# Kernel tuning notes

Hardware: AMD Instinct MI355X
Metric: run time of the kernel (lower is better)

Reference implementation:

```python
import jax, jax.numpy as jnp
import numpy as np

N_NODES = 50000
N_EDGES = 800000
D_IN = 512
D_OUT = 128

def setup_inputs() -> dict:
    key = jax.random.key(0)
    k1, k2, k3, k4, k5, k6 = jax.random.split(key, 6)
    std = 1.0 / np.sqrt(D_OUT)
    x = jax.random.normal(k1, (N_NODES, D_IN), dtype=jnp.float32)
    edge_w = jax.random.uniform(k2, (N_EDGES,), dtype=jnp.float32)
    src = jax.random.randint(k3, (N_EDGES,), 0, N_NODES, dtype=jnp.int32)
    dst = jax.random.randint(k4, (N_EDGES,), 0, N_NODES, dtype=jnp.int32)
    W = jax.random.uniform(k5, (D_IN, D_OUT), minval=-std, maxval=std, dtype=jnp.float32)
    b = jax.random.uniform(k6, (D_OUT,), minval=-std, maxval=std, dtype=jnp.float32)
    return {"x": x, "edge_w": edge_w, "src": src, "dst": dst, "W": W, "b": b}

def reference(x, edge_w, src, dst, W, b):
    # Dense GEMM: [N, D_in] @ [D_in, D_out]
    h = x @ W
    # SpMM with COO adjacency: out[i] = sum_{e: dst[e]==i} edge_w[e] * h[src[e]]
    msg = h[src] * edge_w[:, None]          # [E, D_out]
    agg = jax.ops.segment_sum(msg, dst, num_segments=N_NODES)
    return agg + b
```

## Files before the change

### kernel.cpp

```cpp
#include <hip/hip_runtime.h>
#include <hip/hip_bf16.h>

#define M_NODES  50000
#define D_IN_K   512
#define D_OUT_N  128
#define N_EDGES  800000
#define SCAN_NBLK 49

typedef short  bf16x8 __attribute__((ext_vector_type(8)));
typedef float  f32x4  __attribute__((ext_vector_type(4)));

static __device__ __forceinline__ unsigned short f2bf(float f) {
    unsigned u = __float_as_uint(f);
    unsigned r = u + 0x7FFF + ((u >> 16) & 1);
    return (unsigned short)(r >> 16);
}
static __device__ __forceinline__ float bflo(unsigned q) { return __uint_as_float(q << 16); }
static __device__ __forceinline__ float bfhi(unsigned q) { return __uint_as_float(q & 0xFFFF0000u); }

static __device__ __forceinline__ void gl2lds16(const uint4* g, uint4* l) {
    __builtin_amdgcn_global_load_lds(
        (const __attribute__((address_space(1))) void*)g,
        (__attribute__((address_space(3))) void*)l,
        16, 0, 0);
}

__global__ __launch_bounds__(256) void permw_kernel(const float* __restrict__ W,
                                                    unsigned short* __restrict__ Wp) {
    int tid = blockIdx.x * 256 + threadIdx.x;
    int lane = tid & 63;
    int nt   = (tid >> 6) & 7;
    int kb4  = tid >> 9;
    int n    = nt * 16 + (lane & 15);
    int kbase = kb4 * 32 + ((lane >> 4) & 3) * 8;
    unsigned short frag[8];
#pragma unroll
    for (int j = 0; j < 8; ++j)
        frag[j] = f2bf(W[(size_t)(kbase + j) * D_OUT_N + n]);
    *(uint4*)&Wp[(size_t)tid * 8] = *(const uint4*)frag;
}

__global__ __launch_bounds__(256, 4) void mfma_gemm_hist_kernel(const float* __restrict__ x,
                                                                const uint4* __restrict__ Wp4,
                                                                unsigned short* __restrict__ h,
                                                                const int* __restrict__ dst,
                                                                int* __restrict__ counts) {
    __shared__ uint4 wlds[2][1024];

    const int tid  = threadIdx.x;
    const int wave = tid >> 6;
    const int lane = tid & 63;
    const int m0   = blockIdx.x * 64 + wave * 16;
    const int mrow = lane & 15;
    const int kgrp = lane >> 4;

    const int r0 = m0 + mrow;
    const float* xr0 = x + (size_t)((r0 < M_NODES) ? r0 : M_NODES - 1) * D_IN_K + kgrp * 8;

    f32x4 acc[8];
#pragma unroll
    for (int t = 0; t < 8; ++t) acc[t] = (f32x4){0.f, 0.f, 0.f, 0.f};

#pragma unroll
    for (int i = 0; i < 4; ++i)
        gl2lds16(Wp4 + tid + i * 256, &wlds[0][tid + i * 256]);

    float4 a0 = *(const float4*)(xr0);
    float4 a1 = *(const float4*)(xr0 + 4);

    __syncthreads();

    for (int c = 0; c < 8; ++c) {
        const int pb = c & 1;
        if (c < 7) {
#pragma unroll
            for (int i = 0; i < 4; ++i)
                gl2lds16(Wp4 + (c + 1) * 1024 + tid + i * 256,
                         &wlds[pb ^ 1][tid + i * 256]);
        }
#pragma unroll
        for (int kk = 0; kk < 2; ++kk) {
            const int kb = c * 2 + kk;
            float4 n0, n1;
            if (kb < 15) {
                const float* p = xr0 + (kb + 1) * 32;
                n0 = *(const float4*)(p);
                n1 = *(const float4*)(p + 4);
            }
            union { bf16x8 v; __hip_bfloat162 h2[4]; } cv;
            cv.h2[0] = __float22bfloat162_rn(make_float2(a0.x, a0.y));
            cv.h2[1] = __float22bfloat162_rn(make_float2(a0.z, a0.w));
            cv.h2[2] = __float22bfloat162_rn(make_float2(a1.x, a1.y));
            cv.h2[3] = __float22bfloat162_rn(make_float2(a1.z, a1.w));
            bf16x8 af = cv.v;
#pragma unroll
            for (int nt = 0; nt < 8; ++nt) {
                union { uint4 u; bf16x8 v; } wb;
                wb.u = wlds[pb][kk * 512 + nt * 64 + lane];
                acc[nt] = __builtin_amdgcn_mfma_f32_16x16x32_bf16(af, wb.v, acc[nt], 0, 0, 0);
            }
            if (kb < 15) { a0 = n0; a1 = n1; }
        }
        __syncthreads();
    }

#pragma unroll
    for (int r = 0; r < 4; ++r) {
        int rr = m0 + kgrp * 4 + r;
        if (rr < M_NODES) {
            unsigned short* hp = h + (size_t)rr * D_OUT_N + mrow;
#pragma unroll
            for (int nt = 0; nt < 8; ++nt)
                hp[nt * 16] = f2bf(acc[nt][r]);
        }
    }

    const int epb = (N_EDGES + gridDim.x - 1) / gridDim.x;
    const int e0  = blockIdx.x * epb;
    const int e1  = (e0 + epb < N_EDGES) ? e0 + epb : N_EDGES;
    for (int e = e0 + tid; e < e1; e += 256)
        atomicAdd(&counts[dst[e]], 1);
}

__global__ __launch_bounds__(256) void scan_kernel(const int* __restrict__ counts,
                                                   int* __restrict__ offsets,
                                                   int* __restrict__ cursor,
                                                   int* __restrict__ partials,
                                                   int* __restrict__ flags) {
    __shared__ int wsum[4];
    __shared__ int carry_s;
    const int tid  = threadIdx.x;
    const int lane = tid & 63;
    const int wid  = tid >> 6;
    const int blk  = blockIdx.x;
    const int base = blk * 1024 + tid * 4;

    int v[4];
    if (base + 3 < M_NODES) {
        int4 q = *(const int4*)&counts[base];
        v[0] = q.x; v[1] = q.y; v[2] = q.z; v[3] = q.w;
    } else {
#pragma unroll
        for (int i = 0; i < 4; ++i)
            v[i] = (base + i < M_NODES) ? counts[base + i] : 0;
    }
    int t = v[0] + v[1] + v[2] + v[3];

    int s = t;
#pragma unroll
    for (int d = 1; d < 64; d <<= 1) {
        int u = __shfl_up(s, d, 64);
        if (lane >= d) s += u;
    }
    if (lane == 63) wsum[wid] = s;
    __syncthreads();
    int wbase = 0;
#pragma unroll
    for (int w = 0; w < 4; ++w) wbase += (w < wid) ? wsum[w] : 0;
    int total = wsum[0] + wsum[1] + wsum[2] + wsum[3];

    if (tid == 0) {
        __hip_atomic_store(&partials[blk], total, __ATOMIC_RELAXED, __HIP_MEMORY_SCOPE_AGENT);
        __hip_atomic_store(&flags[blk], 1, __ATOMIC_RELEASE, __HIP_MEMORY_SCOPE_AGENT);
        if (blk == 0) offsets[M_NODES] = N_EDGES;
    }

    if (wid == 0) {
        int val = 0;
        if (lane < blk) {
            while (__hip_atomic_load(&flags[lane], __ATOMIC_ACQUIRE, __HIP_MEMORY_SCOPE_AGENT) == 0) {}
            val = __hip_atomic_load(&partials[lane], __ATOMIC_RELAXED, __HIP_MEMORY_SCOPE_AGENT);
        }
#pragma unroll
        for (int d = 32; d > 0; d >>= 1) val += __shfl_xor(val, d, 64);
        if (lane == 0) carry_s = val;
    }
    __syncthreads();
    const int carry = carry_s;

    int run = carry + wbase + s - t;
#pragma unroll
    for (int i = 0; i < 4; ++i) {
        if (base + i < M_NODES) {
            offsets[base + i] = run;
            cursor[base + i]  = run;
        }
        run += v[i];
    }
}

__global__ __launch_bounds__(256) void fill_kernel(const int* __restrict__ src,
                                                   const int* __restrict__ dst,
                                                   const float* __restrict__ edge_w,
                                                   int* __restrict__ cursor,
                                                   int2* __restrict__ ep) {
    int e = blockIdx.x * blockDim.x + threadIdx.x;
    if (e >= N_EDGES) return;
    int d   = dst[e];
    int pos = atomicAdd(&cursor[d], 1);
    ep[pos] = make_int2(src[e], __float_as_int(edge_w[e]));
}

__global__ __launch_bounds__(256) void gather_kernel(const unsigned short* __restrict__ h,
                                                     const int2* __restrict__ ep,
                                                     const int* __restrict__ offsets,
                                                     const float* __restrict__ b,
                                                     float* __restrict__ out) {
    int t    = blockIdx.x * blockDim.x + threadIdx.x;
    int node = t >> 4;
    int lane = t & 15;
    if (node >= M_NODES) return;
    int beg = offsets[node];
    int end = offsets[node + 1];

    float4 b0 = *(const float4*)&b[lane * 8];
    float4 b1 = *(const float4*)&b[lane * 8 + 4];
    float a[4][8];
#pragma unroll
    for (int u = 0; u < 4; ++u)
#pragma unroll
        for (int c = 0; c < 8; ++c) a[u][c] = 0.f;

    int j = beg;
    for (; j + 4 <= end; j += 4) {
        int2 e0 = ep[j], e1 = ep[j + 1], e2 = ep[j + 2], e3 = ep[j + 3];
        uint4 q0 = *(const uint4*)(h + (size_t)e0.x * D_OUT_N + lane * 8);
        uint4 q1 = *(const uint4*)(h + (size_t)e1.x * D_OUT_N + lane * 8);
        uint4 q2 = *(const uint4*)(h + (size_t)e2.x * D_OUT_N + lane * 8);
        uint4 q3 = *(const uint4*)(h + (size_t)e3.x * D_OUT_N + lane * 8);
        float w0 = __int_as_float(e0.y), w1 = __int_as_float(e1.y);
        float w2 = __int_as_float(e2.y), w3 = __int_as_float(e3.y);
        a[0][0] += w0 * bflo(q0.x);  a[0][1] += w0 * bfhi(q0.x);
        a[0][2] += w0 * bflo(q0.y);  a[0][3] += w0 * bfhi(q0.y);
        a[0][4] += w0 * bflo(q0.z);  a[0][5] += w0 * bfhi(q0.z);
        a[0][6] += w0 * bflo(q0.w);  a[0][7] += w0 * bfhi(q0.w);
        a[1][0] += w1 * bflo(q1.x);  a[1][1] += w1 * bfhi(q1.x);
        a[1][2] += w1 * bflo(q1.y);  a[1][3] += w1 * bfhi(q1.y);
        a[1][4] += w1 * bflo(q1.z);  a[1][5] += w1 * bfhi(q1.z);
        a[1][6] += w1 * bflo(q1.w);  a[1][7] += w1 * bfhi(q1.w);
        a[2][0] += w2 * bflo(q2.x);  a[2][1] += w2 * bfhi(q2.x);
        a[2][2] += w2 * bflo(q2.y);  a[2][3] += w2 * bfhi(q2.y);
        a[2][4] += w2 * bflo(q2.z);  a[2][5] += w2 * bfhi(q2.z);
        a[2][6] += w2 * bflo(q2.w);  a[2][7] += w2 * bfhi(q2.w);
        a[3][0] += w3 * bflo(q3.x);  a[3][1] += w3 * bfhi(q3.x);
        a[3][2] += w3 * bflo(q3.y);  a[3][3] += w3 * bfhi(q3.y);
        a[3][4] += w3 * bflo(q3.z);  a[3][5] += w3 * bfhi(q3.z);
        a[3][6] += w3 * bflo(q3.w);  a[3][7] += w3 * bfhi(q3.w);
    }
    for (; j < end; ++j) {
        int2 e0 = ep[j];
        float w0 = __int_as_float(e0.y);
        uint4 q0 = *(const uint4*)(h + (size_t)e0.x * D_OUT_N + lane * 8);
        a[0][0] += w0 * bflo(q0.x);  a[0][1] += w0 * bfhi(q0.x);
        a[0][2] += w0 * bflo(q0.y);  a[0][3] += w0 * bfhi(q0.y);
        a[0][4] += w0 * bflo(q0.z);  a[0][5] += w0 * bfhi(q0.z);
        a[0][6] += w0 * bflo(q0.w);  a[0][7] += w0 * bfhi(q0.w);
    }

    float4 o0 = make_float4(b0.x + a[0][0] + a[1][0] + a[2][0] + a[3][0],
                            b0.y + a[0][1] + a[1][1] + a[2][1] + a[3][1],
                            b0.z + a[0][2] + a[1][2] + a[2][2] + a[3][2],
                            b0.w + a[0][3] + a[1][3] + a[2][3] + a[3][3]);
    float4 o1 = make_float4(b1.x + a[0][4] + a[1][4] + a[2][4] + a[3][4],
                            b1.y + a[0][5] + a[1][5] + a[2][5] + a[3][5],
                            b1.z + a[0][6] + a[1][6] + a[2][6] + a[3][6],
                            b1.w + a[0][7] + a[1][7] + a[2][7] + a[3][7]);
    float* op = &out[(size_t)node * D_OUT_N + lane * 8];
    *(float4*)op = o0;
    *(float4*)(op + 4) = o1;
}

extern "C" void kernel_launch(void* const* d_in, const int* in_sizes, int n_in,
                              void* d_out, int out_size, void* d_ws, size_t ws_size,
                              hipStream_t stream) {
    const float* x      = (const float*)d_in[0];
    const float* edge_w = (const float*)d_in[1];
    const int*   src    = (const int*)d_in[2];
    const int*   dst    = (const int*)d_in[3];
    const float* W      = (const float*)d_in[4];
    const float* b      = (const float*)d_in[5];
    float* out = (float*)d_out;

    char* wsp = (char*)d_ws;
    unsigned short* h = (unsigned short*)wsp;  wsp += (size_t)M_NODES * D_OUT_N * 2;
    int*   counts   = (int*)wsp;         wsp += (size_t)M_NODES * 4;
    int*   flags    = (int*)wsp;         wsp += 64 * 4;
    int*   cursor   = (int*)wsp;         wsp += (size_t)M_NODES * 4;
    int*   offsets  = (int*)wsp;         wsp += (((size_t)M_NODES + 1) * 4 + 15) & ~15ull;
    int2*  ep       = (int2*)wsp;        wsp += (size_t)N_EDGES * 8;
    unsigned short* Wp = (unsigned short*)wsp; wsp += (size_t)16 * 8 * 64 * 8 * 2;
    int*   partials = (int*)wsp;         wsp += (SCAN_NBLK * 4 + 15) & ~15ull;

    hipMemsetAsync(counts, 0, (size_t)M_NODES * 4 + 64 * 4, stream);
    permw_kernel<<<32, 256, 0, stream>>>(W, Wp);
    mfma_gemm_hist_kernel<<<(M_NODES + 63) / 64, 256, 0, stream>>>(
        x, (const uint4*)Wp, h, dst, counts);
    scan_kernel<<<SCAN_NBLK, 256, 0, stream>>>(counts, offsets, cursor, partials, flags);
    fill_kernel<<<(N_EDGES + 255) / 256, 256, 0, stream>>>(src, dst, edge_w, cursor, ep);
    gather_kernel<<<(int)(((long long)M_NODES * 16 + 255) / 256), 256, 0, stream>>>(
        h, ep, offsets, b, out);
}
```

Before: 293.9 us.

## Load GEMM weight fragments directly into registers instead of LDS double-buffer

```diff
diff --git a/kernel.cpp b/kernel.cpp
--- a/kernel.cpp
+++ b/kernel.cpp
@@ -17,13 +17,6 @@
 }
 static __device__ __forceinline__ float bflo(unsigned q) { return __uint_as_float(q << 16); }
 static __device__ __forceinline__ float bfhi(unsigned q) { return __uint_as_float(q & 0xFFFF0000u); }
-
-static __device__ __forceinline__ void gl2lds16(const uint4* g, uint4* l) {
-    __builtin_amdgcn_global_load_lds(
-        (const __attribute__((address_space(1))) void*)g,
-        (__attribute__((address_space(3))) void*)l,
-        16, 0, 0);
-}
 
 __global__ __launch_bounds__(256) void permw_kernel(const float* __restrict__ W,
                                                     unsigned short* __restrict__ Wp) {
@@ -40,13 +33,11 @@
     *(uint4*)&Wp[(size_t)tid * 8] = *(const uint4*)frag;
 }
 
-__global__ __launch_bounds__(256, 4) void mfma_gemm_hist_kernel(const float* __restrict__ x,
+__global__ __launch_bounds__(256, 3) void mfma_gemm_hist_kernel(const float* __restrict__ x,
                                                                 const uint4* __restrict__ Wp4,
                                                                 unsigned short* __restrict__ h,
                                                                 const int* __restrict__ dst,
                                                                 int* __restrict__ counts) {
-    __shared__ uint4 wlds[2][1024];
-
     const int tid  = threadIdx.x;
     const int wave = tid >> 6;
     const int lane = tid & 63;
@@ -61,47 +52,45 @@
 #pragma unroll
     for (int t = 0; t < 8; ++t) acc[t] = (f32x4){0.f, 0.f, 0.f, 0.f};
 
-#pragma unroll
-    for (int i = 0; i < 4; ++i)
-        gl2lds16(Wp4 + tid + i * 256, &wlds[0][tid + i * 256]);
-
+    const uint4* wp = Wp4 + lane;
+
+    uint4 wcur[8], wnxt[8];
+#pragma unroll
+    for (int nt = 0; nt < 8; ++nt) wcur[nt] = wp[nt * 64];
     float4 a0 = *(const float4*)(xr0);
     float4 a1 = *(const float4*)(xr0 + 4);
 
-    __syncthreads();
-
-    for (int c = 0; c < 8; ++c) {
-        const int pb = c & 1;
-        if (c < 7) {
-#pragma unroll
-            for (int i = 0; i < 4; ++i)
-                gl2lds16(Wp4 + (c + 1) * 1024 + tid + i * 256,
-                         &wlds[pb ^ 1][tid + i * 256]);
-        }
-#pragma unroll
-        for (int kk = 0; kk < 2; ++kk) {
-            const int kb = c * 2 + kk;
-            float4 n0, n1;
-            if (kb < 15) {
-                const float* p = xr0 + (kb + 1) * 32;
-                n0 = *(const float4*)(p);
-                n1 = *(const float4*)(p + 4);
-            }
-            union { bf16x8 v; __hip_bfloat162 h2[4]; } cv;
-            cv.h2[0] = __float22bfloat162_rn(make_float2(a0.x, a0.y));
-            cv.h2[1] = __float22bfloat162_rn(make_float2(a0.z, a0.w));
-            cv.h2[2] = __float22bfloat162_rn(make_float2(a1.x, a1.y));
-            cv.h2[3] = __float22bfloat162_rn(make_float2(a1.z, a1.w));
-            bf16x8 af = cv.v;
-#pragma unroll
-            for (int nt = 0; nt < 8; ++nt) {
-                union { uint4 u; bf16x8 v; } wb;
-                wb.u = wlds[pb][kk * 512 + nt * 64 + lane];
-                acc[nt] = __builtin_amdgcn_mfma_f32_16x16x32_bf16(af, wb.v, acc[nt], 0, 0, 0);
-            }
-            if (kb < 15) { a0 = n0; a1 = n1; }
-        }
-        __syncthreads();
+#pragma unroll 2
+    for (int kb = 0; kb < 16; ++kb) {
+        float4 n0, n1;
+        if (kb < 15) {
+#pragma unroll
+            for (int nt = 0; nt < 8; ++nt)
+                wnxt[nt] = wp[(kb + 1) * 512 + nt * 64];
+            const float* p = xr0 + (kb + 1) * 32;
+            n0 = *(const float4*)(p);
+            n1 = *(const float4*)(p + 4);
+        }
+
+        union { bf16x8 v; __hip_bfloat162 h2[4]; } cv;
+        cv.h2[0] = __float22bfloat162_rn(make_float2(a0.x, a0.y));
+        cv.h2[1] = __float22bfloat162_rn(make_float2(a0.z, a0.w));
+        cv.h2[2] = __float22bfloat162_rn(make_float2(a1.x, a1.y));
+        cv.h2[3] = __float22bfloat162_rn(make_float2(a1.z, a1.w));
+        bf16x8 af = cv.v;
+
+#pragma unroll
+        for (int nt = 0; nt < 8; ++nt) {
+            union { uint4 u; bf16x8 v; } wb;
+            wb.u = wcur[nt];
+            acc[nt] = __builtin_amdgcn_mfma_f32_16x16x32_bf16(af, wb.v, acc[nt], 0, 0, 0);
+        }
+
+        if (kb < 15) {
+#pragma unroll
+            for (int nt = 0; nt < 8; ++nt) wcur[nt] = wnxt[nt];
+            a0 = n0; a1 = n1;
+        }
     }
 
 #pragma unroll
```

After: 307.1 us. 4.5% more time.
